# Optimization experiments

Measured on AMD Instinct MI355X. Metric: run time of the kernel, lower is better.

The kernel has to match this reference:

```python
import jax, jax.numpy as jnp
import numpy as np

TEMP = 0.07
LAMBDA_CON = 1.0
LAMBDA_SHELL = 1.0
NEG_INF = -1e30


def setup_inputs() -> dict:
    key = jax.random.key(0)
    k1, k2, k3, k4, k5 = jax.random.split(key, 5)
    B, D = 8192, 1024
    emb = jax.random.normal(k1, (B, D), jnp.float32)
    emb = emb / jnp.linalg.norm(emb, axis=1, keepdims=True)  # encoder outputs are unit-norm
    center = jax.random.normal(k2, (D,), jnp.float32)
    center = center / jnp.linalg.norm(center)  # buffer is F.normalize'd in estimate_epoch_geometry
    labels = jax.random.randint(k3, (B,), 0, 2)  # 0 = machine, 1 = human
    radius_m = jax.random.uniform(k4, (1,), jnp.float32)
    radius_h = radius_m + jax.random.uniform(k5, (1,), jnp.float32)  # radius_h >= radius_m by construction
    return {"embeddings": emb, "center": center, "radius_m": radius_m,
            "radius_h": radius_h, "labels": labels}


def reference(embeddings, center, radius_m, radius_h, labels):
    rm = radius_m[0]
    rh = radius_h[0]
    B = embeddings.shape[0]

    # ---- shell loss ----
    distances = jnp.linalg.norm(embeddings - center[None, :], axis=1)  # [B]
    mmask = labels == 0
    hmask = labels == 1
    nm = jnp.sum(mmask)
    nh = jnp.sum(hmask)
    loss_m = jnp.sum(jnp.where(mmask, jnp.square(jax.nn.relu(distances - rm)), 0.0)) / jnp.maximum(nm, 1)
    loss_h = jnp.sum(jnp.where(hmask, jnp.square(jax.nn.relu(rh - distances)), 0.0)) / jnp.maximum(nh, 1)
    loss_shell = loss_m + loss_h

    # ---- contrastive loss (batched: one BxB sim matrix instead of per-anchor loop) ----
    S = (embeddings @ embeddings.T) / TEMP          # [B, B] pairwise logits
    Sp = (embeddings @ center) / TEMP               # [B]  logits vs prototype
    eye = jnp.eye(B, dtype=bool)
    S_masked = jnp.where(eye, jnp.asarray(NEG_INF, S.dtype), S)
    # denominator per machine anchor i: logsumexp over {other machines, prototype, humans}
    # (labels are only 0/1, so all j != i contribute) plus the prototype logit
    lse = jnp.logaddexp(jax.nn.logsumexp(S_masked, axis=1), Sp)  # [B]
    # positives for machine anchor i: other machines (nm-1) + prototype -> nm positives
    pos_sum = jnp.sum(jnp.where(mmask[None, :] & ~eye, S, 0.0), axis=1) + Sp  # [B]
    anchor_loss = lse - pos_sum / jnp.maximum(nm, 1)
    con_sum = jnp.sum(jnp.where(mmask, anchor_loss, 0.0))
    # prototype as anchor: positives = machines, negatives = humans
    lse_p = jax.nn.logsumexp(Sp)
    proto_loss = lse_p - jnp.sum(jnp.where(mmask, Sp, 0.0)) / jnp.maximum(nm, 1)
    loss_con = (con_sum + proto_loss) / jnp.maximum(nm + 1, 1)
    # original returns 0 when either class is empty
    both = (nm > 0) & (nh > 0)
    loss_con = jnp.where(both, loss_con, 0.0)

    loss = LAMBDA_SHELL * loss_shell + LAMBDA_CON * loss_con
    return (loss, loss_shell, loss_m, loss_h, loss_con, distances)
```

## Files before the change

### kernel.cpp

```cpp
#include <hip/hip_runtime.h>

#define INV_T 14.285714285714286f
#define C1 0.055803571428571425f

typedef float f32x16 __attribute__((ext_vector_type(16)));
typedef float f32x4 __attribute__((ext_vector_type(4)));
typedef int i32x4v __attribute__((ext_vector_type(4)));
typedef int i32x8 __attribute__((ext_vector_type(8)));

__device__ __forceinline__ unsigned char f2e4m3(float f) {
    unsigned char s = (unsigned char)((__float_as_uint(f) >> 24) & 0x80);
    float a = fabsf(f);
    if (a > 448.f) a = 448.f;
    if (a == 0.f) return s;
    int e = (int)((__float_as_uint(a) >> 23) & 0xFF) - 127;
    if (e < -10) return s;
    if (e < -6) e = -6;
    float scale = __int_as_float((unsigned)(130 - e) << 23);
    int mi = (int)rintf(a * scale);
    if (mi >= 16) { mi >>= 1; ++e; }
    if (mi < 8) return s | (unsigned char)mi;
    return s | (unsigned char)(((e + 7) << 3) | (mi - 8));
}

__device__ __forceinline__ void async16(void* l, const void* g) {
    __builtin_amdgcn_global_load_lds(
        (const __attribute__((address_space(1))) unsigned int*)g,
        (__attribute__((address_space(3))) unsigned int*)l, 16, 0, 0);
}

__global__ void __launch_bounds__(256) k_geom(const float* __restrict__ emb,
                                              const float* __restrict__ center,
                                              const int* __restrict__ labels,
                                              float* __restrict__ out,
                                              float* __restrict__ Sp,
                                              float* __restrict__ s_mp,
                                              int D) {
    int t = threadIdx.x;
    int wave = t >> 6, lane = t & 63;
    int nw = blockDim.x >> 6;
    int r0 = blockIdx.x * 16;
    float4 c = ((const float4*)center)[t];
    float d2p[16], spp[16];
    float4 colacc = {0.f, 0.f, 0.f, 0.f};
#pragma unroll
    for (int g = 0; g < 2; ++g) {
        int rbase = r0 + g * 8;
        float4 e[8];
#pragma unroll
        for (int r = 0; r < 8; ++r)
            e[r] = ((const float4*)(emb + (size_t)(rbase + r) * D))[t];
        int lab[8];
#pragma unroll
        for (int r = 0; r < 8; ++r) lab[r] = labels[rbase + r];
#pragma unroll
        for (int r = 0; r < 8; ++r) {
            float sc = (lab[r] == 0) ? 1.f : 0.f;
            float dx = e[r].x - c.x, dy = e[r].y - c.y,
                  dz = e[r].z - c.z, dw = e[r].w - c.w;
            d2p[g * 8 + r] = dx * dx + dy * dy + dz * dz + dw * dw;
            spp[g * 8 + r] = e[r].x * c.x + e[r].y * c.y + e[r].z * c.z + e[r].w * c.w;
            colacc.x += e[r].x * sc; colacc.y += e[r].y * sc;
            colacc.z += e[r].z * sc; colacc.w += e[r].w * sc;
        }
    }
#pragma unroll
    for (int m = 1; m <= 32; m <<= 1)
#pragma unroll
        for (int r = 0; r < 16; ++r) {
            d2p[r] += __shfl_xor(d2p[r], m, 64);
            spp[r] += __shfl_xor(spp[r], m, 64);
        }
    __shared__ float redD[16][4];
    __shared__ float redS[16][4];
    if (lane == 0)
#pragma unroll
        for (int r = 0; r < 16; ++r) { redD[r][wave] = d2p[r]; redS[r][wave] = spp[r]; }

    ((float4*)(s_mp + (size_t)blockIdx.x * D))[t] = colacc;

    __syncthreads();
    if (t < 16) {
        float d2 = 0.f, sp = 0.f;
        for (int w = 0; w < nw; ++w) { d2 += redD[t][w]; sp += redS[t][w]; }
        out[5 + r0 + t] = sqrtf(d2);
        Sp[r0 + t] = sp * INV_T;
    }
}

__global__ void __launch_bounds__(256) k_quant(const float* __restrict__ emb,
                                               unsigned char* __restrict__ embQ,
                                               float* __restrict__ sumexp,
                                               float* __restrict__ scal,
                                               unsigned* __restrict__ done_ctr,
                                               int D) {
    int t = threadIdx.x;
    int r0 = blockIdx.x * 8;
    if (t < 8) sumexp[blockIdx.x * 8 + t] = 0.f;
    if (blockIdx.x == 0) {
        if (t < 12) scal[t] = 0.f;
        if (t == 12) *done_ctr = 0u;
    }
    float4 e[8];
#pragma unroll
    for (int r = 0; r < 8; ++r)
        e[r] = ((const float4*)(emb + (size_t)(r0 + r) * D))[t];
#pragma unroll
    for (int r = 0; r < 8; ++r) {
#if __has_builtin(__builtin_amdgcn_cvt_pk_fp8_f32)
        int p = 0;
        p = __builtin_amdgcn_cvt_pk_fp8_f32(e[r].x * 16.f, e[r].y * 16.f, p, false);
        p = __builtin_amdgcn_cvt_pk_fp8_f32(e[r].z * 16.f, e[r].w * 16.f, p, true);
        ((int*)(embQ + (size_t)(r0 + r) * D))[t] = p;
#else
        ((uchar4*)(embQ + (size_t)(r0 + r) * D))[t] =
            make_uchar4(f2e4m3(e[r].x * 16.f), f2e4m3(e[r].y * 16.f),
                        f2e4m3(e[r].z * 16.f), f2e4m3(e[r].w * 16.f));
#endif
    }
}

#define MXMFMA(a, b, c) __builtin_amdgcn_mfma_scale_f32_32x32x64_f8f6f4( \
    (a), (b), (c), 0, 0, 0, 0x7F7F7F7F, 0, 0x7F7F7F7F)

__global__ void __launch_bounds__(256, 2)
k_sumexp_mx(const unsigned char* __restrict__ embQ, float* __restrict__ sumexp,
            int D, int nT) {
    const int n = nT;
    int bid = blockIdx.x;
    float nf = (float)n + 0.5f;
    int rb = (int)(nf - sqrtf(fmaxf(nf * nf - 2.0f * (float)bid, 0.f)));
    if (rb < 0) rb = 0;
    if (rb > n - 1) rb = n - 1;
#define TRI_OFF(r) ((r) * n - ((r) * ((r)-1)) / 2)
    while (rb + 1 <= n - 1 && TRI_OFF(rb + 1) <= bid) ++rb;
    while (rb > 0 && TRI_OFF(rb) > bid) --rb;
    int cb = rb + (bid - TRI_OFF(rb));
#undef TRI_OFF
    int rowbase = rb * 128, colbase = cb * 128;

    int tid = threadIdx.x;
    int wave = tid >> 6, lane = tid & 63;
    int wr = wave >> 1, wc = wave & 1;
    int l31 = lane & 31, kk = lane >> 5;

    __shared__ unsigned char sA[2][16384];
    __shared__ unsigned char sB[2][16384];
    __shared__ float rred[2][128];
    __shared__ float cred[2][128];

    f32x16 acc[2][2];
#pragma unroll
    for (int fr = 0; fr < 2; ++fr)
#pragma unroll
        for (int fc = 0; fc < 2; ++fc)
#pragma unroll
            for (int v = 0; v < 16; ++v) acc[fr][fc][v] = 0.f;

    const int kG = D >> 7;

    const unsigned char* gSA[4];
    const unsigned char* gSB[4];
    unsigned int dstOff[4];
#pragma unroll
    for (int q = 0; q < 4; ++q) {
        int ch = q * 256 + tid;
        int row = ch >> 3, lc = ch & 7;
        int gc = lc ^ (row & 7);
        gSA[q] = embQ + (size_t)(rowbase + row) * D + gc * 16;
        gSB[q] = embQ + (size_t)(colbase + row) * D + gc * 16;
        dstOff[q] = (unsigned)ch << 4;
    }

    auto stage = [&](int buf, int kt) {
        int ko = kt << 7;
#pragma unroll
        for (int q = 0; q < 4; ++q) {
            async16(&sA[buf][dstOff[q]], gSA[q] + ko);
            async16(&sB[buf][dstOff[q]], gSB[q] + ko);
        }
    };

    int e7 = (l31 & 7) << 4;
    int offs[2][2];
#pragma unroll
    for (int h = 0; h < 2; ++h)
#pragma unroll
        for (int j = 0; j < 2; ++j)
            offs[h][j] = (((h * 4 + kk * 2 + j) << 4) ^ e7);
    int aBase0 = (wr * 64 + l31) << 7;
    int aBase1 = aBase0 + (32 << 7);
    int bBase0 = (wc * 64 + l31) << 7;
    int bBase1 = bBase0 + (32 << 7);

    stage(0, 0);
    for (int kt = 0; kt < kG; ++kt) {
        int cur = kt & 1;
        __syncthreads();
        if (kt + 1 < kG) stage(cur ^ 1, kt + 1);
        const unsigned char* A = sA[cur];
        const unsigned char* Bp = sB[cur];
#pragma unroll
        for (int h = 0; h < 2; ++h) {
            i32x8 av[2], bv[2];
            {
                i32x4v lo = *(const i32x4v*)&A[aBase0 + offs[h][0]];
                i32x4v hi = *(const i32x4v*)&A[aBase0 + offs[h][1]];
                av[0] = __builtin_shufflevector(lo, hi, 0, 1, 2, 3, 4, 5, 6, 7);
            }
            {
                i32x4v lo = *(const i32x4v*)&A[aBase1 + offs[h][0]];
                i32x4v hi = *(const i32x4v*)&A[aBase1 + offs[h][1]];
                av[1] = __builtin_shufflevector(lo, hi, 0, 1, 2, 3, 4, 5, 6, 7);
            }
            {
                i32x4v lo = *(const i32x4v*)&Bp[bBase0 + offs[h][0]];
                i32x4v hi = *(const i32x4v*)&Bp[bBase0 + offs[h][1]];
                bv[0] = __builtin_shufflevector(lo, hi, 0, 1, 2, 3, 4, 5, 6, 7);
            }
            {
                i32x4v lo = *(const i32x4v*)&Bp[bBase1 + offs[h][0]];
                i32x4v hi = *(const i32x4v*)&Bp[bBase1 + offs[h][1]];
                bv[1] = __builtin_shufflevector(lo, hi, 0, 1, 2, 3, 4, 5, 6, 7);
            }
#pragma unroll
            for (int fr = 0; fr < 2; ++fr)
#pragma unroll
                for (int fc = 0; fc < 2; ++fc)
                    acc[fr][fc] = MXMFMA(av[fr], bv[fc], acc[fr][fc]);
        }
    }

    float rs[2][16];
    float cs[2] = {0.f, 0.f};
#pragma unroll
    for (int fr = 0; fr < 2; ++fr)
#pragma unroll
        for (int v = 0; v < 16; ++v) rs[fr][v] = 0.f;

#pragma unroll
    for (int fr = 0; fr < 2; ++fr)
#pragma unroll
        for (int fc = 0; fc < 2; ++fc) {
            int gcol = colbase + wc * 64 + fc * 32 + l31;
#pragma unroll
            for (int v = 0; v < 16; ++v) {
                int grow = rowbase + wr * 64 + fr * 32 + (v & 3) + 8 * (v >> 2) + 4 * kk;
                float e = (grow < gcol) ? __expf(acc[fr][fc][v] * C1 - INV_T) : 0.f;
                rs[fr][v] += e;
                cs[fc] += e;
            }
        }

#pragma unroll
    for (int m = 1; m <= 16; m <<= 1)
#pragma unroll
        for (int fr = 0; fr < 2; ++fr)
#pragma unroll
            for (int v = 0; v < 16; ++v) rs[fr][v] += __shfl_xor(rs[fr][v], m, 64);
    if (l31 == 0)
#pragma unroll
        for (int fr = 0; fr < 2; ++fr)
#pragma unroll
            for (int v = 0; v < 16; ++v)
                rred[wc][wr * 64 + fr * 32 + (v & 3) + 8 * (v >> 2) + 4 * kk] = rs[fr][v];

#pragma unroll
    for (int fc = 0; fc < 2; ++fc) cs[fc] += __shfl_xor(cs[fc], 32, 64);
    if (kk == 0)
#pragma unroll
        for (int fc = 0; fc < 2; ++fc) cred[wr][wc * 64 + fc * 32 + l31] = cs[fc];

    __syncthreads();
    if (tid < 128) {
        atomicAdd(&sumexp[rowbase + tid], rred[0][tid] + rred[1][tid]);
    } else {
        int u = tid - 128;
        atomicAdd(&sumexp[colbase + u], cred[0][u] + cred[1][u]);
    }
}

typedef __bf16 bf16x8 __attribute__((ext_vector_type(8)));
typedef unsigned short u16x8 __attribute__((ext_vector_type(8)));
__device__ __forceinline__ unsigned short f2bf(float f) {
    unsigned int x = __float_as_uint(f);
    x += 0x7fffu + ((x >> 16) & 1u);
    return (unsigned short)(x >> 16);
}
__global__ void __launch_bounds__(256) k_sumexp_fb(const float* __restrict__ embF,
                                                   float* __restrict__ sumexp, int D, int nTiles) {
    int bid = blockIdx.x;
    const int n = nTiles;
    float nf = (float)n + 0.5f;
    int rb = (int)(nf - sqrtf(fmaxf(nf * nf - 2.0f * (float)bid, 0.f)));
    if (rb < 0) rb = 0;
    if (rb > n - 1) rb = n - 1;
#define TRI_OFF(r) ((r) * n - ((r) * ((r)-1)) / 2)
    while (rb + 1 <= n - 1 && TRI_OFF(rb + 1) <= bid) ++rb;
    while (rb > 0 && TRI_OFF(rb) > bid) --rb;
    int cb = rb + (bid - TRI_OFF(rb));
#undef TRI_OFF
    int tid = threadIdx.x;
    int wave = tid >> 6, lane = tid & 63;
    int wr = wave >> 1, wc = wave & 1;
    int quad = lane >> 4, l15 = lane & 15;
    int rowbase = rb * 128, colbase = cb * 128;
    __shared__ unsigned short lA[128 * 64];
    __shared__ unsigned short lB[128 * 64];
    __shared__ float rred[2][128];
    __shared__ float cred[2][128];
    f32x4 zero = {0.f, 0.f, 0.f, 0.f};
    f32x4 acc[4][4];
#pragma unroll
    for (int r = 0; r < 4; ++r)
#pragma unroll
        for (int c = 0; c < 4; ++c) acc[r][c] = zero;
    const int kIters = D >> 6;
    for (int kt = 0; kt < kIters; ++kt) {
        int k0 = kt << 6;
#pragma unroll
        for (int q = 0; q < 4; ++q) {
            int ch = q * 256 + tid;
            int row = ch >> 3, lc = ch & 7;
            int pc = lc ^ (row & 7);
            const float4* sa = (const float4*)(embF + (size_t)(rowbase + row) * D + k0 + lc * 8);
            const float4* sb = (const float4*)(embF + (size_t)(colbase + row) * D + k0 + lc * 8);
            float4 a0 = sa[0], a1 = sa[1];
            float4 b0 = sb[0], b1 = sb[1];
            u16x8 va = {f2bf(a0.x), f2bf(a0.y), f2bf(a0.z), f2bf(a0.w),
                        f2bf(a1.x), f2bf(a1.y), f2bf(a1.z), f2bf(a1.w)};
            u16x8 vb = {f2bf(b0.x), f2bf(b0.y), f2bf(b0.z), f2bf(b0.w),
                        f2bf(b1.x), f2bf(b1.y), f2bf(b1.z), f2bf(b1.w)};
            *(u16x8*)&lA[(row << 6) + (pc << 3)] = va;
            *(u16x8*)&lB[(row << 6) + (pc << 3)] = vb;
        }
        __syncthreads();
#pragma unroll
        for (int h = 0; h < 2; ++h) {
            bf16x8 af[4], bfr[4];
#pragma unroll
            for (int r = 0; r < 4; ++r) {
                int row = wr * 64 + r * 16 + l15;
                int pc = (h * 4 + quad) ^ (l15 & 7);
                af[r] = *(const bf16x8*)&lA[(row << 6) + (pc << 3)];
            }
#pragma unroll
            for (int c = 0; c < 4; ++c) {
                int row = wc * 64 + c * 16 + l15;
                int pc = (h * 4 + quad) ^ (l15 & 7);
                bfr[c] = *(const bf16x8*)&lB[(row << 6) + (pc << 3)];
            }
#pragma unroll
            for (int r = 0; r < 4; ++r)
#pragma unroll
                for (int c = 0; c < 4; ++c)
                    acc[r][c] = __builtin_amdgcn_mfma_f32_16x16x32_bf16(af[r], bfr[c], acc[r][c], 0, 0, 0);
        }
        __syncthreads();
    }
    float rs[4][4], cs[4];
#pragma unroll
    for (int r = 0; r < 4; ++r)
#pragma unroll
        for (int v = 0; v < 4; ++v) rs[r][v] = 0.f;
#pragma unroll
    for (int c = 0; c < 4; ++c) cs[c] = 0.f;
#pragma unroll
    for (int r = 0; r < 4; ++r)
#pragma unroll
        for (int c = 0; c < 4; ++c) {
            f32x4 a = acc[r][c];
            int gcol = colbase + wc * 64 + c * 16 + l15;
#pragma unroll
            for (int v = 0; v < 4; ++v) {
                int grow = rowbase + wr * 64 + r * 16 + quad * 4 + v;
                float e = (grow < gcol) ? __expf((a[v] - 1.0f) * INV_T) : 0.f;
                rs[r][v] += e;
                cs[c] += e;
            }
        }
#pragma unroll
    for (int m = 1; m <= 8; m <<= 1)
#pragma unroll
        for (int r = 0; r < 4; ++r)
#pragma unroll
            for (int v = 0; v < 4; ++v) rs[r][v] += __shfl_xor(rs[r][v], m, 64);
    if (l15 == 0)
#pragma unroll
        for (int r = 0; r < 4; ++r)
#pragma unroll
            for (int v = 0; v < 4; ++v)
                rred[wc][wr * 64 + r * 16 + quad * 4 + v] = rs[r][v];
#pragma unroll
    for (int m = 16; m <= 32; m <<= 1)
#pragma unroll
        for (int c = 0; c < 4; ++c) cs[c] += __shfl_xor(cs[c], m, 64);
    if (quad == 0)
#pragma unroll
        for (int c = 0; c < 4; ++c) cred[wr][wc * 64 + c * 16 + l15] = cs[c];
    __syncthreads();
    if (tid < 128) {
        atomicAdd(&sumexp[rowbase + tid], rred[0][tid] + rred[1][tid]);
    } else {
        int u = tid & 127;
        atomicAdd(&sumexp[colbase + u], cred[0][u] + cred[1][u]);
    }
}

__global__ void __launch_bounds__(256) k_fin(const float* __restrict__ Sp,
                                             const float* __restrict__ sumexp,
                                             const int* __restrict__ labels,
                                             const float* __restrict__ outv,
                                             const float* __restrict__ s_mp,
                                             const float* __restrict__ center,
                                             const float* __restrict__ rmp,
                                             const float* __restrict__ rhp,
                                             float* __restrict__ scal,
                                             unsigned* __restrict__ done_ctr,
                                             float* __restrict__ out,
                                             int D, int B, int nPart) {
    int t = threadIdx.x, lane = t & 63, wave = t >> 6;
    int i = blockIdx.x * blockDim.x + t;
    float rm = rmp[0], rh = rhp[0];
    float a[9];
#pragma unroll
    for (int k = 0; k < 9; ++k) a[k] = 0.f;
    if (i < B) {
        float LP = Sp[i];
        float eS = __expf(LP - INV_T);
        float lse = INV_T + __logf(sumexp[i] + eS);
        float d = outv[5 + i];
        bool mach = (labels[i] == 0);
        a[2] = eS;
        if (mach) {
            a[4] = lse; a[3] = LP; a[5] = d * d; a[8] = 1.f;
            float x = d - rm; a[0] = (x > 0.f) ? x * x : 0.f;
        } else {
            float x = rh - d; a[1] = (x > 0.f) ? x * x : 0.f;
        }
    }
    if (blockIdx.x == 0)
        for (int j = t; j < D; j += blockDim.x) { float cv = center[j]; a[7] += cv * cv; }
    __shared__ float sacc[8][33];
    int pg = t >> 5, dl = t & 31;
    for (int dbase = blockIdx.x * 32; dbase < D; dbase += gridDim.x * 32) {
        int d = dbase + dl;
        float a0 = 0.f, a1 = 0.f, a2 = 0.f, a3 = 0.f;
        if (d < D) {
            for (int p = pg; p < nPart; p += 32) {
                a0 += s_mp[(size_t)p * D + d];
                a1 += s_mp[(size_t)(p + 8) * D + d];
                a2 += s_mp[(size_t)(p + 16) * D + d];
                a3 += s_mp[(size_t)(p + 24) * D + d];
            }
        }
        sacc[pg][dl] = (a0 + a1) + (a2 + a3);
        __syncthreads();
        if (t < 32 && dbase + t < D) {
            float s = sacc[0][t] + sacc[1][t] + sacc[2][t] + sacc[3][t] +
                      sacc[4][t] + sacc[5][t] + sacc[6][t] + sacc[7][t];
            a[6] += s * s;
        }
        __syncthreads();
    }
#pragma unroll
    for (int m = 1; m <= 32; m <<= 1)
#pragma unroll
        for (int k = 0; k < 9; ++k) a[k] += __shfl_xor(a[k], m, 64);
    __shared__ float red[4][9];
    if (lane == 0)
#pragma unroll
        for (int k = 0; k < 9; ++k) red[wave][k] = a[k];
    __syncthreads();
    if (t < 9) {
        float v = red[0][t] + red[1][t] + red[2][t] + red[3][t];
        atomicAdd(&scal[t], v);
    }
    __syncthreads();
    if (t == 0) {
        __threadfence();
        unsigned done = atomicAdd(done_ctr, 1u);
        if (done == (unsigned)gridDim.x - 1) {
            __threadfence();
            float s[9];
#pragma unroll
            for (int k = 0; k < 9; ++k) s[k] = atomicAdd(&scal[k], 0.f);
            int nm = (int)(s[8] + 0.5f);
            int nh = B - nm;
            float nmf = (float)(nm > 1 ? nm : 1);
            float nhf = (float)(nh > 1 ? nh : 1);
            float loss_m = s[0] / nmf;
            float loss_h = s[1] / nhf;
            float loss_shell = loss_m + loss_h;
            float lse_p = INV_T + __logf(s[2]);
            float proto = lse_p - s[3] / nmf;
            float sum_sd = s[5] + 2.f * s[3] / INV_T - (float)nm * s[7];
            float pos_m = INV_T * (s[6] - sum_sd) + s[3];
            float con = s[4] - pos_m / nmf;
            int denom = (nm + 1 > 1) ? nm + 1 : 1;
            float lc = (con + proto) / (float)denom;
            if (!(nm > 0 && nh > 0)) lc = 0.f;
            out[0] = loss_shell + lc;
            out[1] = loss_shell;
            out[2] = loss_m;
            out[3] = loss_h;
            out[4] = lc;
        }
    }
}

extern "C" void kernel_launch(void* const* d_in, const int* in_sizes, int n_in,
                              void* d_out, int out_size, void* d_ws, size_t ws_size,
                              hipStream_t stream) {
    const float* emb = (const float*)d_in[0];
    const float* center = (const float*)d_in[1];
    const float* rmp = (const float*)d_in[2];
    const float* rhp = (const float*)d_in[3];
    const int* labels = (const int*)d_in[4];
    float* out = (float*)d_out;
    const int B = in_sizes[4];
    const int D = in_sizes[1];

    const int nPart = B / 16;
    size_t qBytes = (size_t)B * D;
    size_t partBytes = (size_t)nPart * D * 4;
    size_t auxBytes = (size_t)B * 4 + 64 + (size_t)B * 4 + partBytes;
    bool pre = (ws_size >= qBytes + auxBytes) && (B % 256 == 0) &&
               (D % 256 == 0) && (D <= 1024);
    size_t Z0 = pre ? qBytes : 0;

    char* ws = (char*)d_ws;
    unsigned char* embQ = (unsigned char*)ws;
    float* sumexp = (float*)(ws + Z0);
    float* scal = (float*)(ws + Z0 + (size_t)B * 4);
    unsigned* done_ctr = (unsigned*)(scal + 12);
    float* Sp = (float*)(ws + Z0 + (size_t)B * 4 + 64);
    float* s_mp = (float*)(ws + Z0 + (size_t)B * 4 + 64 + (size_t)B * 4);

    k_geom<<<B / 16, D / 4, 0, stream>>>(emb, center, labels, out, Sp, s_mp, D);

    if (pre) {
        k_quant<<<B / 8, D / 4, 0, stream>>>(emb, embQ, sumexp, scal, done_ctr, D);
    } else {
        hipMemsetAsync(ws + Z0, 0, (size_t)B * 4 + 64, stream);
    }

    int nT = B / 128;
    int nBlocks = nT * (nT + 1) / 2;
    if (pre) k_sumexp_mx<<<nBlocks, 256, 0, stream>>>(embQ, sumexp, D, nT);
    else     k_sumexp_fb<<<nBlocks, 256, 0, stream>>>(emb, sumexp, D, nT);

    k_fin<<<(B + 255) / 256, 256, 0, stream>>>(Sp, sumexp, labels, out, s_mp,
                                               center, rmp, rhp, scal,
                                               done_ctr, out, D, B, nPart);
}
```

Before: 171.6 us.

## Switch Gram-matrix sumexp from MX-FP8 to BF16 MFMA and fuse conversion into geom

Replaces the FP8 (e4m3 scaled MFMA 32x32x64) similarity pass with a BF16 MFMA 32x32x16 path, so the embedding matrix is staged at twice the byte width and the K loop runs twice as many iterations. The separate quantization kernel is removed: the BF16 conversion and the zeroing of the sumexp, scalar and counter buffers now happen inside k_geom, which already reads the embeddings. This saves a launch and a full re-read of the input, but doubles the operand bytes and matrix-instruction count in the dominant kernel. The likely motivation is accuracy or robustness rather than raw throughput.

Measured after the change: 210.0 us. 1.22x slower.

```diff
diff --git a/kernel.cpp b/kernel.cpp
--- a/kernel.cpp
+++ b/kernel.cpp
@@ -1,26 +1,16 @@
 #include <hip/hip_runtime.h>
 
 #define INV_T 14.285714285714286f
-#define C1 0.055803571428571425f
 
 typedef float f32x16 __attribute__((ext_vector_type(16)));
 typedef float f32x4 __attribute__((ext_vector_type(4)));
-typedef int i32x4v __attribute__((ext_vector_type(4)));
-typedef int i32x8 __attribute__((ext_vector_type(8)));
-
-__device__ __forceinline__ unsigned char f2e4m3(float f) {
-    unsigned char s = (unsigned char)((__float_as_uint(f) >> 24) & 0x80);
-    float a = fabsf(f);
-    if (a > 448.f) a = 448.f;
-    if (a == 0.f) return s;
-    int e = (int)((__float_as_uint(a) >> 23) & 0xFF) - 127;
-    if (e < -10) return s;
-    if (e < -6) e = -6;
-    float scale = __int_as_float((unsigned)(130 - e) << 23);
-    int mi = (int)rintf(a * scale);
-    if (mi >= 16) { mi >>= 1; ++e; }
-    if (mi < 8) return s | (unsigned char)mi;
-    return s | (unsigned char)(((e + 7) << 3) | (mi - 8));
+typedef __bf16 bf16x8 __attribute__((ext_vector_type(8)));
+typedef unsigned short u16x8 __attribute__((ext_vector_type(8)));
+
+__device__ __forceinline__ unsigned short f2bf(float f) {
+    unsigned int x = __float_as_uint(f);
+    x += 0x7fffu + ((x >> 16) & 1u);
+    return (unsigned short)(x >> 16);
 }
 
 __device__ __forceinline__ void async16(void* l, const void* g) {
@@ -35,11 +25,23 @@
                                               float* __restrict__ out,
                                               float* __restrict__ Sp,
                                               float* __restrict__ s_mp,
+                                              unsigned char* __restrict__ embB,
+                                              float* __restrict__ sumexp,
+                                              float* __restrict__ scal,
+                                              unsigned* __restrict__ done_ctr,
                                               int D) {
     int t = threadIdx.x;
     int wave = t >> 6, lane = t & 63;
     int nw = blockDim.x >> 6;
     int r0 = blockIdx.x * 16;
+    const size_t pitch = (size_t)D * 2;
+
+    if (t < 16) sumexp[blockIdx.x * 16 + t] = 0.f;
+    if (blockIdx.x == 0) {
+        if (t < 12) scal[t] = 0.f;
+        if (t == 12) *done_ctr = 0u;
+    }
+
     float4 c = ((const float4*)center)[t];
     float d2p[16], spp[16];
     float4 colacc = {0.f, 0.f, 0.f, 0.f};
@@ -53,6 +55,14 @@
         int lab[8];
 #pragma unroll
         for (int r = 0; r < 8; ++r) lab[r] = labels[rbase + r];
+        if (embB) {
+#pragma unroll
+            for (int r = 0; r < 8; ++r) {
+                ushort4 p = make_ushort4(f2bf(e[r].x), f2bf(e[r].y),
+                                         f2bf(e[r].z), f2bf(e[r].w));
+                ((ushort4*)(embB + (size_t)(rbase + r) * pitch))[t] = p;
+            }
+        }
 #pragma unroll
         for (int r = 0; r < 8; ++r) {
             float sc = (lab[r] == 0) ? 1.f : 0.f;
@@ -88,43 +98,8 @@
     }
 }
 
-__global__ void __launch_bounds__(256) k_quant(const float* __restrict__ emb,
-                                               unsigned char* __restrict__ embQ,
-                                               float* __restrict__ sumexp,
-                                               float* __restrict__ scal,
-                                               unsigned* __restrict__ done_ctr,
-                                               int D) {
-    int t = threadIdx.x;
-    int r0 = blockIdx.x * 8;
-    if (t < 8) sumexp[blockIdx.x * 8 + t] = 0.f;
-    if (blockIdx.x == 0) {
-        if (t < 12) scal[t] = 0.f;
-        if (t == 12) *done_ctr = 0u;
-    }
-    float4 e[8];
-#pragma unroll
-    for (int r = 0; r < 8; ++r)
-        e[r] = ((const float4*)(emb + (size_t)(r0 + r) * D))[t];
-#pragma unroll
-    for (int r = 0; r < 8; ++r) {
-#if __has_builtin(__builtin_amdgcn_cvt_pk_fp8_f32)
-        int p = 0;
-        p = __builtin_amdgcn_cvt_pk_fp8_f32(e[r].x * 16.f, e[r].y * 16.f, p, false);
-        p = __builtin_amdgcn_cvt_pk_fp8_f32(e[r].z * 16.f, e[r].w * 16.f, p, true);
-        ((int*)(embQ + (size_t)(r0 + r) * D))[t] = p;
-#else
-        ((uchar4*)(embQ + (size_t)(r0 + r) * D))[t] =
-            make_uchar4(f2e4m3(e[r].x * 16.f), f2e4m3(e[r].y * 16.f),
-                        f2e4m3(e[r].z * 16.f), f2e4m3(e[r].w * 16.f));
-#endif
-    }
-}
-
-#define MXMFMA(a, b, c) __builtin_amdgcn_mfma_scale_f32_32x32x64_f8f6f4( \
-    (a), (b), (c), 0, 0, 0, 0x7F7F7F7F, 0, 0x7F7F7F7F)
-
 __global__ void __launch_bounds__(256, 2)
-k_sumexp_mx(const unsigned char* __restrict__ embQ, float* __restrict__ sumexp,
+k_sumexp_bf(const unsigned char* __restrict__ embB, float* __restrict__ sumexp,
             int D, int nT) {
     const int n = nT;
     int bid = blockIdx.x;
@@ -143,6 +118,7 @@
     int wave = tid >> 6, lane = tid & 63;
     int wr = wave >> 1, wc = wave & 1;
     int l31 = lane & 31, kk = lane >> 5;
+    const size_t pitch = (size_t)D * 2;
 
     __shared__ unsigned char sA[2][16384];
     __shared__ unsigned char sB[2][16384];
@@ -157,7 +133,7 @@
 #pragma unroll
             for (int v = 0; v < 16; ++v) acc[fr][fc][v] = 0.f;
 
-    const int kG = D >> 7;
+    const int kIters = D >> 6;
 
     const unsigned char* gSA[4];
     const unsigned char* gSB[4];
@@ -167,8 +143,8 @@
         int ch = q * 256 + tid;
         int row = ch >> 3, lc = ch & 7;
         int gc = lc ^ (row & 7);
-        gSA[q] = embQ + (size_t)(rowbase + row) * D + gc * 16;
-        gSB[q] = embQ + (size_t)(colbase + row) * D + gc * 16;
+        gSA[q] = embB + (size_t)(rowbase + row) * pitch + gc * 16;
+        gSB[q] = embB + (size_t)(colbase + row) * pitch + gc * 16;
         dstOff[q] = (unsigned)ch << 4;
     }
 
@@ -181,53 +157,35 @@
         }
     };
 
-    int e7 = (l31 & 7) << 4;
-    int offs[2][2];
-#pragma unroll
-    for (int h = 0; h < 2; ++h)
-#pragma unroll
-        for (int j = 0; j < 2; ++j)
-            offs[h][j] = (((h * 4 + kk * 2 + j) << 4) ^ e7);
-    int aBase0 = (wr * 64 + l31) << 7;
-    int aBase1 = aBase0 + (32 << 7);
-    int bBase0 = (wc * 64 + l31) << 7;
-    int bBase1 = bBase0 + (32 << 7);
+    int aOff[2][4], bOff[2][4];
+#pragma unroll
+    for (int f = 0; f < 2; ++f) {
+        int ra = wr * 64 + f * 32 + l31;
+        int rbv = wc * 64 + f * 32 + l31;
+#pragma unroll
+        for (int ks = 0; ks < 4; ++ks) {
+            aOff[f][ks] = ra * 128 + (((2 * ks + kk) ^ (ra & 7)) << 4);
+            bOff[f][ks] = rbv * 128 + (((2 * ks + kk) ^ (rbv & 7)) << 4);
+        }
+    }
 
     stage(0, 0);
-    for (int kt = 0; kt < kG; ++kt) {
+    for (int kt = 0; kt < kIters; ++kt) {
         int cur = kt & 1;
         __syncthreads();
-        if (kt + 1 < kG) stage(cur ^ 1, kt + 1);
+        if (kt + 1 < kIters) stage(cur ^ 1, kt + 1);
         const unsigned char* A = sA[cur];
         const unsigned char* Bp = sB[cur];
 #pragma unroll
-        for (int h = 0; h < 2; ++h) {
-            i32x8 av[2], bv[2];
-            {
-                i32x4v lo = *(const i32x4v*)&A[aBase0 + offs[h][0]];
-                i32x4v hi = *(const i32x4v*)&A[aBase0 + offs[h][1]];
-                av[0] = __builtin_shufflevector(lo, hi, 0, 1, 2, 3, 4, 5, 6, 7);
-            }
-            {
-                i32x4v lo = *(const i32x4v*)&A[aBase1 + offs[h][0]];
-                i32x4v hi = *(const i32x4v*)&A[aBase1 + offs[h][1]];
-                av[1] = __builtin_shufflevector(lo, hi, 0, 1, 2, 3, 4, 5, 6, 7);
-            }
-            {
-                i32x4v lo = *(const i32x4v*)&Bp[bBase0 + offs[h][0]];
-                i32x4v hi = *(const i32x4v*)&Bp[bBase0 + offs[h][1]];
-                bv[0] = __builtin_shufflevector(lo, hi, 0, 1, 2, 3, 4, 5, 6, 7);
-            }
-            {
-                i32x4v lo = *(const i32x4v*)&Bp[bBase1 + offs[h][0]];
-                i32x4v hi = *(const i32x4v*)&Bp[bBase1 + offs[h][1]];
-                bv[1] = __builtin_shufflevector(lo, hi, 0, 1, 2, 3, 4, 5, 6, 7);
-            }
-#pragma unroll
-            for (int fr = 0; fr < 2; ++fr)
-#pragma unroll
-                for (int fc = 0; fc < 2; ++fc)
-                    acc[fr][fc] = MXMFMA(av[fr], bv[fc], acc[fr][fc]);
+        for (int ks = 0; ks < 4; ++ks) {
+            bf16x8 av0 = *(const bf16x8*)&A[aOff[0][ks]];
+            bf16x8 av1 = *(const bf16x8*)&A[aOff[1][ks]];
+            bf16x8 bv0 = *(const bf16x8*)&Bp[bOff[0][ks]];
+            bf16x8 bv1 = *(const bf16x8*)&Bp[bOff[1][ks]];
+            acc[0][0] = __builtin_amdgcn_mfma_f32_32x32x16_bf16(av0, bv0, acc[0][0], 0, 0, 0);
+            acc[0][1] = __builtin_amdgcn_mfma_f32_32x32x16_bf16(av0, bv1, acc[0][1], 0, 0, 0);
+            acc[1][0] = __builtin_amdgcn_mfma_f32_32x32x16_bf16(av1, bv0, acc[1][0], 0, 0, 0);
+            acc[1][1] = __builtin_amdgcn_mfma_f32_32x32x16_bf16(av1, bv1, acc[1][1], 0, 0, 0);
         }
     }
 
@@ -246,7 +204,7 @@
 #pragma unroll
             for (int v = 0; v < 16; ++v) {
                 int grow = rowbase + wr * 64 + fr * 32 + (v & 3) + 8 * (v >> 2) + 4 * kk;
-                float e = (grow < gcol) ? __expf(acc[fr][fc][v] * C1 - INV_T) : 0.f;
+                float e = (grow < gcol) ? __expf(acc[fr][fc][v] * INV_T - INV_T) : 0.f;
                 rs[fr][v] += e;
                 cs[fc] += e;
             }
@@ -280,13 +238,6 @@
     }
 }
 
-typedef __bf16 bf16x8 __attribute__((ext_vector_type(8)));
-typedef unsigned short u16x8 __attribute__((ext_vector_type(8)));
-__device__ __forceinline__ unsigned short f2bf(float f) {
-    unsigned int x = __float_as_uint(f);
-    x += 0x7fffu + ((x >> 16) & 1u);
-    return (unsigned short)(x >> 16);
-}
 __global__ void __launch_bounds__(256) k_sumexp_fb(const float* __restrict__ embF,
                                                    float* __restrict__ sumexp, int D, int nTiles) {
     int bid = blockIdx.x;
@@ -522,32 +473,28 @@
     const int D = in_sizes[1];
 
     const int nPart = B / 16;
-    size_t qBytes = (size_t)B * D;
+    size_t bBytes = (size_t)B * D * 2;
     size_t partBytes = (size_t)nPart * D * 4;
     size_t auxBytes = (size_t)B * 4 + 64 + (size_t)B * 4 + partBytes;
-    bool pre = (ws_size >= qBytes + auxBytes) && (B % 256 == 0) &&
+    bool pre = (ws_size >= bBytes + auxBytes) && (B % 256 == 0) &&
                (D % 256 == 0) && (D <= 1024);
-    size_t Z0 = pre ? qBytes : 0;
+    size_t Z0 = pre ? bBytes : 0;
 
     char* ws = (char*)d_ws;
-    unsigned char* embQ = (unsigned char*)ws;
+    unsigned char* embB = (unsigned char*)ws;
     float* sumexp = (float*)(ws + Z0);
     float* scal = (float*)(ws + Z0 + (size_t)B * 4);
     unsigned* done_ctr = (unsigned*)(scal + 12);
     float* Sp = (float*)(ws + Z0 + (size_t)B * 4 + 64);
     float* s_mp = (float*)(ws + Z0 + (size_t)B * 4 + 64 + (size_t)B * 4);
 
-    k_geom<<<B / 16, D / 4, 0, stream>>>(emb, center, labels, out, Sp, s_mp, D);
-
-    if (pre) {
-        k_quant<<<B / 8, D / 4, 0, stream>>>(emb, embQ, sumexp, scal, done_ctr, D);
-    } else {
-        hipMemsetAsync(ws + Z0, 0, (size_t)B * 4 + 64, stream);
-    }
+    k_geom<<<B / 16, D / 4, 0, stream>>>(emb, center, labels, out, Sp, s_mp,
+                                         pre ? embB : nullptr, sumexp, scal,
+                                         done_ctr, D);
 
     int nT = B / 128;
     int nBlocks = nT * (nT + 1) / 2;
-    if (pre) k_sumexp_mx<<<nBlocks, 256, 0, stream>>>(embQ, sumexp, D, nT);
+    if (pre) k_sumexp_bf<<<nBlocks, 256, 0, stream>>>(embB, sumexp, D, nT);
     else     k_sumexp_fb<<<nBlocks, 256, 0, stream>>>(emb, sumexp, D, nT);
 
     k_fin<<<(B + 255) / 256, 256, 0, stream>>>(Sp, sumexp, labels, out, s_mp,
```
